# Kernel tuning notes

Hardware: AMD Instinct MI355X
Metric: run time of the kernel (lower is better)

The kernel has to match this reference:

```python
import jax, jax.numpy as jnp
import numpy as np

B, CL, QL, D2 = 64, 1024, 128, 512  # batch, c_len, q_len, hidden_size*2


def setup_inputs() -> dict:
    key = jax.random.key(0)
    ks = jax.random.split(key, 6)
    scale = 1.0 / np.sqrt(D2)
    return {
        "c": jax.random.normal(ks[0], (B, CL, D2), jnp.float32),
        "q": jax.random.normal(ks[1], (B, QL, D2), jnp.float32),
        "w_c": jax.random.normal(ks[2], (D2,), jnp.float32) * scale,
        "b_c": jnp.zeros((1,), jnp.float32),
        "w_q": jax.random.normal(ks[3], (D2,), jnp.float32) * scale,
        "b_q": jnp.zeros((1,), jnp.float32),
        "w_cq": jax.random.normal(ks[4], (D2,), jnp.float32) * scale,
        "b_cq": jnp.zeros((1,), jnp.float32),
    }


def reference(c, q, w_c, b_c, w_q, b_q, w_cq, b_cq):
    # BiDAF trilinear similarity.
    # Source loops over q_len: att_weight_cq(c * q_i); equivalent to
    # cq[b,i,j] = sum_d c[b,i,d] * q[b,j,d] * w_cq[d] + b_cq  -> single batched matmul.
    s_c = c @ w_c + b_c  # [B, CL]
    s_q = q @ w_q + b_q  # [B, QL]
    cq = jnp.einsum("bid,bjd->bij", c * w_cq, q) + b_cq  # [B, CL, QL]
    s = s_c[:, :, None] + s_q[:, None, :] + cq  # [B, CL, QL]
    a = jax.nn.softmax(s, axis=2)
    c2q = jnp.einsum("bij,bjd->bid", a, q)  # context-to-query attention
    b_att = jax.nn.softmax(jnp.max(s, axis=2), axis=1)  # [B, CL]
    q2c = jnp.einsum("bi,bid->bd", b_att, c)[:, None, :]  # [B, 1, D2], broadcast over CL
    x = jnp.concatenate([c, c2q, c * c2q, c * q2c], axis=-1)  # [B, CL, 8H]
    return x
```

## Files before the change

kernel.cpp:

```cpp
#include <hip/hip_runtime.h>

using bf16x8 = __attribute__((ext_vector_type(8))) short;
using f32x4  = __attribute__((ext_vector_type(4))) float;

#define NB 64
#define CLN 1024
#define QLN 128
#define DDN 512

typedef __attribute__((address_space(1))) const void GAS;
typedef __attribute__((address_space(3))) void LAS;

__device__ __forceinline__ unsigned short f2bf(float x){
    union { float f; unsigned u; } v; v.f = x;
    unsigned r = v.u + 0x7FFFu + ((v.u >> 16) & 1u);
    return (unsigned short)(r >> 16);
}
__device__ __forceinline__ float bf2f(unsigned short u){
    union { unsigned u; float f; } v; v.u = ((unsigned)u) << 16; return v.f;
}

__global__ __launch_bounds__(256) void k0_qprep(const float* __restrict__ q,
        unsigned short* __restrict__ qT, unsigned short* __restrict__ qbf){
    __shared__ float tile[QLN][65];
    const int b  = blockIdx.x;
    const int d0 = blockIdx.y * 64;
    const int t  = threadIdx.x;
    {
        const int col = t & 63, rg = t >> 6;
        #pragma unroll 4
        for (int p = 0; p < 32; ++p){
            int j = p*4 + rg;
            float v = q[(size_t)(b*QLN + j)*DDN + d0 + col];
            tile[j][col] = v;
            qbf[(size_t)(b*QLN + j)*DDN + d0 + col] = f2bf(v);
        }
    }
    __syncthreads();
    {
        const int j = t & 127, dg = t >> 7;
        #pragma unroll 4
        for (int p = 0; p < 32; ++p){
            int dd = p*2 + dg;
            qT[(size_t)(b*DDN + d0 + dd)*QLN + j] = f2bf(tile[j][dd]);
        }
    }
}

__global__ __launch_bounds__(256) void k0b_sq(const float* __restrict__ q,
        const float* __restrict__ w_q, float* __restrict__ sq){
    const int b = blockIdx.x;
    const int t = threadIdx.x;
    const int wave = t >> 6, lane = t & 63;
    float wv[8];
    #pragma unroll
    for (int e=0;e<8;++e) wv[e] = w_q[lane*8+e];
    for (int j = wave; j < QLN; j += 4){
        const float* qr = q + (size_t)(b*QLN + j)*DDN + lane*8;
        float s = 0.f;
        #pragma unroll
        for (int e=0;e<8;++e) s += qr[e]*wv[e];
        #pragma unroll
        for (int m=1;m<64;m<<=1) s += __shfl_xor(s, m, 64);
        if (lane==0) sq[b*QLN + j] = s;
    }
}

__global__ __launch_bounds__(256) void k0c_cprep(const float* __restrict__ c,
        const float* __restrict__ w_c, const float* __restrict__ w_cq,
        float* out, float* __restrict__ sc_ws, float* __restrict__ inv_ws){
    const int t = threadIdx.x, lane = t & 63, w = t >> 6;
    const int row0 = blockIdx.x*32 + w*8;
    float4 wc0 = *(const float4*)(w_c  + lane*8);
    float4 wc1 = *(const float4*)(w_c  + lane*8 + 4);
    float4 wq0 = *(const float4*)(w_cq + lane*8);
    float4 wq1 = *(const float4*)(w_cq + lane*8 + 4);
    #pragma unroll 2
    for (int p=0;p<8;++p){
        const size_t gi = (size_t)(row0 + p);
        const float* cr = c + gi*DDN + lane*8;
        f32x4 a  = *(const f32x4*)cr;
        f32x4 bb = *(const f32x4*)(cr+4);
        float s = a.x*wc0.x + a.y*wc0.y + a.z*wc0.z + a.w*wc0.w
                + bb.x*wc1.x + bb.y*wc1.y + bb.z*wc1.z + bb.w*wc1.w;
        #pragma unroll
        for (int m=1;m<64;m<<=1) s += __shfl_xor(s, m, 64);
        float* orow = out + gi*2048;
        __builtin_nontemporal_store(a,  (f32x4*)(orow + lane*8));
        __builtin_nontemporal_store(bb, (f32x4*)(orow + lane*8 + 4));
        uint4 pk;
        pk.x = (unsigned)f2bf(a.x*wq0.x)  | ((unsigned)f2bf(a.y*wq0.y)  << 16);
        pk.y = (unsigned)f2bf(a.z*wq0.z)  | ((unsigned)f2bf(a.w*wq0.w)  << 16);
        pk.z = (unsigned)f2bf(bb.x*wq1.x) | ((unsigned)f2bf(bb.y*wq1.y) << 16);
        pk.w = (unsigned)f2bf(bb.z*wq1.z) | ((unsigned)f2bf(bb.w*wq1.w) << 16);
        *(uint4*)((unsigned short*)(orow + 1792) + lane*8) = pk;
        if (lane==0) sc_ws[gi] = s;
    }
    if (blockIdx.x == 0){
        for (int d=t; d<DDN; d+=256){
            float wv = w_cq[d];
            inv_ws[d] = (fabsf(wv) > 1e-35f) ? 1.0f/wv : 0.0f;
        }
    }
}

__device__ __forceinline__ void stage_tile(const float* out, size_t girow0, int kc,
        unsigned short* buf, int wm, int lane){
    const int rsub = lane >> 3, c16 = lane & 7;
    #pragma unroll
    for (int r=0;r<4;++r){
        const int chunk = wm*4 + r;
        const int row   = chunk*8 + rsub;
        const int col16 = c16 ^ (row & 7);
        const unsigned short* g =
            (const unsigned short*)(out + (girow0 + row)*2048 + 1792) + kc*64 + col16*8;
        __builtin_amdgcn_global_load_lds((GAS*)g, (LAS*)(buf + chunk*512), 16, 0, 0);
    }
}

__global__ __launch_bounds__(256,3) void k1_main(
        float* out, const unsigned short* __restrict__ qbf,
        const unsigned short* __restrict__ qT, const float* __restrict__ sq_ws,
        const float* __restrict__ sc_ws, const float* __restrict__ inv_ws,
        float* __restrict__ vts, float* __restrict__ Mts, float* __restrict__ Sts){
    __shared__ unsigned short sm_u[16384];
    __shared__ float sm_vw[4][512];
    __shared__ float sm_sc[128], sm_sq[128], sm_m[128], sm_red[8];

    const int bid  = blockIdx.x;
    const int swzb = (bid & 7)*64 + (bid >> 3);
    const int b    = swzb >> 3;
    const int tile = swzb & 7;
    const int i0   = tile * 128;
    const int t    = threadIdx.x;
    const int lane = t & 63;
    const int wm   = t >> 6;
    const int l15  = lane & 15;
    const int l4   = lane >> 4;
    const size_t girow0 = (size_t)(b*CLN + i0);

    if (t < 128){ sm_sc[t] = sc_ws[girow0 + t]; sm_sq[t] = sq_ws[b*QLN + t]; }

    f32x4 acc[2][8];
    #pragma unroll
    for (int mi=0;mi<2;++mi)
        #pragma unroll
        for (int ni=0;ni<8;++ni) acc[mi][ni] = f32x4{0.f,0.f,0.f,0.f};

    stage_tile(out, girow0, 0, sm_u, wm, lane);
    __syncthreads();
    const unsigned short* qbbase = qbf + (size_t)b*QLN*DDN;
    for (int kc=0; kc<8; ++kc){
        const int cur = kc & 1;
        if (kc < 7) stage_tile(out, girow0, kc+1, sm_u + (cur^1)*8192, wm, lane);
        const char* abase = (const char*)sm_u + cur*16384;
        #pragma unroll
        for (int ks=0; ks<2; ++ks){
            const int kk2 = (ks*32 + l4*8)*2;
            bf16x8 af[2], bfr[8];
            #pragma unroll
            for (int mi=0;mi<2;++mi){
                const int row = wm*32 + mi*16 + l15;
                af[mi] = *(const bf16x8*)(abase + row*128 + (kk2 ^ ((row&7)<<4)));
            }
            #pragma unroll
            for (int ni=0;ni<8;++ni)
                bfr[ni] = *(const bf16x8*)(qbbase + (size_t)(ni*16+l15)*DDN + kc*64 + ks*32 + l4*8);
            #pragma unroll
            for (int mi=0;mi<2;++mi)
                #pragma unroll
                for (int ni=0;ni<8;++ni)
                    acc[mi][ni] = __builtin_amdgcn_mfma_f32_16x16x32_bf16(af[mi], bfr[ni], acc[mi][ni], 0,0,0);
        }
        __syncthreads();
    }

    float sqv[8];
    #pragma unroll
    for (int ni=0;ni<8;++ni) sqv[ni] = sm_sq[ni*16 + l15];
    #pragma unroll
    for (int mi=0;mi<2;++mi){
        #pragma unroll
        for (int r=0;r<4;++r){
            float rmax = -1e30f;
            #pragma unroll
            for (int ni=0;ni<8;++ni){
                float v = acc[mi][ni][r] + sqv[ni];
                acc[mi][ni][r] = v;
                rmax = fmaxf(rmax, v);
            }
            #pragma unroll
            for (int m=1;m<16;m<<=1) rmax = fmaxf(rmax, __shfl_xor(rmax, m, 64));
            const int iloc = wm*32 + mi*16 + l4*4 + r;
            if (l15 == 0) sm_m[iloc] = sm_sc[iloc] + rmax;
            float rsum = 0.f;
            #pragma unroll
            for (int ni=0;ni<8;++ni){
                float pv = __expf(acc[mi][ni][r] - rmax);
                acc[mi][ni][r] = pv;
                rsum += pv;
            }
            #pragma unroll
            for (int m=1;m<16;m<<=1) rsum += __shfl_xor(rsum, m, 64);
            const float inv = 1.f / rsum;
            #pragma unroll
            for (int ni=0;ni<8;++ni){
                const int colb = (ni*16 + l15)*2;
                *(unsigned short*)((char*)sm_u + iloc*256 + (colb ^ ((iloc&7)<<4)))
                    = f2bf(acc[mi][ni][r] * inv);
            }
        }
    }
    __syncthreads();

    float e0 = -1e30f;
    if (t < 128) e0 = sm_m[t];
    float v0 = e0;
    #pragma unroll
    for (int m=1;m<64;m<<=1) v0 = fmaxf(v0, __shfl_xor(v0, m, 64));
    if (lane==0) sm_red[wm] = v0;
    __syncthreads();
    const float mt = fmaxf(sm_red[0], sm_red[1]);
    float es = (t < 128) ? __expf(sm_m[t] - mt) : 0.f;
    #pragma unroll
    for (int m=1;m<64;m<<=1) es += __shfl_xor(es, m, 64);
    if (lane==0) sm_red[4+wm] = es;
    __syncthreads();
    const float St = sm_red[4]+sm_red[5]+sm_red[6]+sm_red[7];

    float wrow[2][4];
    #pragma unroll
    for (int mi=0;mi<2;++mi)
        #pragma unroll
        for (int r=0;r<4;++r)
            wrow[mi][r] = __expf(sm_m[wm*32 + mi*16 + l4*4 + r] - mt);
    #pragma unroll
    for (int k=0;k<8;++k) sm_vw[wm][lane + k*64] = 0.f;

    const unsigned short* qtbase = qT + (size_t)b*DDN*QLN;
    for (int dc=0; dc<4; ++dc){
        f32x4 acc2[2][8];
        #pragma unroll
        for (int mi=0;mi<2;++mi)
            #pragma unroll
            for (int ni=0;ni<8;++ni) acc2[mi][ni] = f32x4{0.f,0.f,0.f,0.f};
        #pragma unroll
        for (int jh=0; jh<2; ++jh){
            #pragma unroll
            for (int ks=0; ks<2; ++ks){
                const int kkp2 = (jh*64 + ks*32 + l4*8)*2;
                bf16x8 af[2], bfr[8];
                #pragma unroll
                for (int mi=0;mi<2;++mi){
                    const int row = wm*32 + mi*16 + l15;
                    af[mi] = *(const bf16x8*)((const char*)sm_u + row*256 + (kkp2 ^ ((row&7)<<4)));
                }
                #pragma unroll
                for (int ni=0;ni<8;++ni)
                    bfr[ni] = *(const bf16x8*)(qtbase + (size_t)(dc*128 + ni*16 + l15)*QLN + jh*64 + ks*32 + l4*8);
                #pragma unroll
                for (int mi=0;mi<2;++mi)
                    #pragma unroll
                    for (int ni=0;ni<8;++ni)
                        acc2[mi][ni] = __builtin_amdgcn_mfma_f32_16x16x32_bf16(af[mi], bfr[ni], acc2[mi][ni], 0,0,0);
            }
        }
        float invw[8];
        #pragma unroll
        for (int ni=0;ni<8;++ni) invw[ni] = inv_ws[dc*128 + ni*16 + l15];
        float vpart[8];
        #pragma unroll
        for (int ni=0;ni<8;++ni) vpart[ni] = 0.f;
        #pragma unroll
        for (int mi=0;mi<2;++mi){
            #pragma unroll
            for (int r=0;r<4;++r){
                const int rl = wm*32 + mi*16 + l4*4 + r;
                const unsigned short* cb =
                    (const unsigned short*)(out + (girow0 + rl)*2048 + 1792) + dc*128;
                float* orow = out + (girow0 + rl)*2048;
                const float wgt = wrow[mi][r];
                #pragma unroll
                for (int ni=0;ni<8;++ni){
                    const int dl = ni*16 + l15;
                    const float cv = bf2f(cb[dl]) * invw[ni];
                    const float v  = acc2[mi][ni][r];
                    __builtin_nontemporal_store(v,    orow + 512  + dc*128 + dl);
                    __builtin_nontemporal_store(cv*v, orow + 1024 + dc*128 + dl);
                    vpart[ni] += wgt * cv;
                }
            }
        }
        #pragma unroll
        for (int ni=0;ni<8;++ni){
            float v = vpart[ni];
            v += __shfl_xor(v, 16, 64);
            v += __shfl_xor(v, 32, 64);
            if (l4 == 0) sm_vw[wm][dc*128 + ni*16 + l15] = v;
        }
    }
    __syncthreads();
    for (int d=t; d<DDN; d+=256){
        float v = sm_vw[0][d] + sm_vw[1][d] + sm_vw[2][d] + sm_vw[3][d];
        vts[(size_t)(b*8 + tile)*DDN + d] = v;
    }
    if (t == 0){ Mts[b*8 + tile] = mt; Sts[b*8 + tile] = St; }
}

__global__ __launch_bounds__(256) void k2_combine(const float* __restrict__ vts,
        const float* __restrict__ Mts, const float* __restrict__ Sts,
        float* __restrict__ q2c){
    const int b = blockIdx.x, t = threadIdx.x;
    float Mt[8]; float M = -1e30f;
    #pragma unroll
    for (int i=0;i<8;++i){ Mt[i] = Mts[b*8+i]; M = fmaxf(M, Mt[i]); }
    float coef[8]; float denom = 0.f;
    #pragma unroll
    for (int i=0;i<8;++i){ coef[i] = __expf(Mt[i]-M); denom += coef[i]*Sts[b*8+i]; }
    const float inv = 1.f/denom;
    for (int d=t; d<DDN; d+=256){
        float s = 0.f;
        #pragma unroll
        for (int i=0;i<8;++i) s += coef[i]*vts[(size_t)(b*8+i)*DDN + d];
        q2c[b*DDN + d] = s*inv;
    }
}

__global__ __launch_bounds__(256) void k3_cq2c(float* out,
        const float* __restrict__ q2c, const float* __restrict__ inv_ws){
    const int t = threadIdx.x;
    const int rloc = t >> 6, ch = t & 63;
    for (int pass=0; pass<8; ++pass){
        const size_t rb = (size_t)blockIdx.x + (size_t)pass*2048;
        const size_t gi = rb*4 + rloc;
        const int b = (int)(gi >> 10);
        const unsigned short* cb = (const unsigned short*)(out + gi*2048 + 1792) + ch*8;
        uint4 raw = *(const uint4*)cb;
        const float* qp = q2c + b*DDN + ch*8;
        float4 qa = *(const float4*)qp;
        float4 qb = *(const float4*)(qp+4);
        const float* ip = inv_ws + ch*8;
        float4 ia = *(const float4*)ip;
        float4 ib = *(const float4*)(ip+4);
        f32x4 o0, o1;
        o0.x = bf2f((unsigned short)(raw.x & 0xffff)) * ia.x * qa.x;
        o0.y = bf2f((unsigned short)(raw.x >> 16))    * ia.y * qa.y;
        o0.z = bf2f((unsigned short)(raw.y & 0xffff)) * ia.z * qa.z;
        o0.w = bf2f((unsigned short)(raw.y >> 16))    * ia.w * qa.w;
        o1.x = bf2f((unsigned short)(raw.z & 0xffff)) * ib.x * qb.x;
        o1.y = bf2f((unsigned short)(raw.z >> 16))    * ib.y * qb.y;
        o1.z = bf2f((unsigned short)(raw.w & 0xffff)) * ib.z * qb.z;
        o1.w = bf2f((unsigned short)(raw.w >> 16))    * ib.w * qb.w;
        __syncthreads();
        f32x4* wp = (f32x4*)(out + gi*2048 + 1536) + ch*2;
        __builtin_nontemporal_store(o0, wp);
        __builtin_nontemporal_store(o1, wp+1);
    }
}

extern "C" void kernel_launch(void* const* d_in, const int* in_sizes, int n_in,
                              void* d_out, int out_size, void* d_ws, size_t ws_size,
                              hipStream_t stream) {
    const float* c    = (const float*)d_in[0];
    const float* q    = (const float*)d_in[1];
    const float* w_c  = (const float*)d_in[2];
    const float* w_q  = (const float*)d_in[4];
    const float* w_cq = (const float*)d_in[6];
    float* out = (float*)d_out;

    char* ws = (char*)d_ws;
    unsigned short* qT  = (unsigned short*)ws;
    unsigned short* qbf = (unsigned short*)(ws + 8388608);
    float* sq  = (float*)(ws + 16777216);
    float* sc  = (float*)(ws + 16777216 + 32768);
    float* inv = (float*)(ws + 16777216 + 32768 + 262144);
    float* Mts = (float*)(ws + 16777216 + 32768 + 262144 + 2048);
    float* Sts = (float*)(ws + 16777216 + 32768 + 262144 + 4096);
    float* vts = (float*)(ws + 16777216 + 32768 + 262144 + 6144);
    float* q2c = (float*)(ws + 16777216 + 32768 + 262144 + 6144 + 1048576);

    k0_qprep<<<dim3(NB, 8), 256, 0, stream>>>(q, qT, qbf);
    k0b_sq<<<NB, 256, 0, stream>>>(q, w_q, sq);
    k0c_cprep<<<2048, 256, 0, stream>>>(c, w_c, w_cq, out, sc, inv);
    k1_main<<<NB*8, 256, 0, stream>>>(out, qbf, qT, sq, sc, inv, vts, Mts, Sts);
    k2_combine<<<NB, 256, 0, stream>>>(vts, Mts, Sts, q2c);
    k3_cq2c<<<2048, 256, 0, stream>>>(out, q2c, inv);
}
```

Measured before the change: 266.2 us.

## Fuse context prep into main attention kernel and read fp32 c directly

Removes the separate c-prep kernel: the main kernel now loads fp32 c rows itself, computes the c·w_c score and the bf16 c*w_cq tile in registers, and writes them into LDS with double buffering. The bf16 scratch stash in the output buffer and the reciprocal-weight reconstruction go away. The c2q epilogue reads c exactly in fp32 and also writes the c slice of the output. The final q2c kernel reads fp32 c from the output and uses a flat grid-stride loop. MFMA operand order is swapped so epilogue stores are vectorised float4, at the cost of lower occupancy (launch bound 2) and more LDS.

```diff
diff --git a/kernel.cpp b/kernel.cpp
--- a/kernel.cpp
+++ b/kernel.cpp
@@ -11,10 +11,10 @@
 typedef __attribute__((address_space(1))) const void GAS;
 typedef __attribute__((address_space(3))) void LAS;
 
-__device__ __forceinline__ unsigned short f2bf(float x){
+__device__ __forceinline__ unsigned f2bf(float x){
     union { float f; unsigned u; } v; v.f = x;
     unsigned r = v.u + 0x7FFFu + ((v.u >> 16) & 1u);
-    return (unsigned short)(r >> 16);
+    return r >> 16;
 }
 __device__ __forceinline__ float bf2f(unsigned short u){
     union { unsigned u; float f; } v; v.u = ((unsigned)u) << 16; return v.f;
@@ -33,7 +33,7 @@
             int j = p*4 + rg;
             float v = q[(size_t)(b*QLN + j)*DDN + d0 + col];
             tile[j][col] = v;
-            qbf[(size_t)(b*QLN + j)*DDN + d0 + col] = f2bf(v);
+            qbf[(size_t)(b*QLN + j)*DDN + d0 + col] = (unsigned short)f2bf(v);
         }
     }
     __syncthreads();
@@ -42,7 +42,7 @@
         #pragma unroll 4
         for (int p = 0; p < 32; ++p){
             int dd = p*2 + dg;
-            qT[(size_t)(b*DDN + d0 + dd)*QLN + j] = f2bf(tile[j][dd]);
+            qT[(size_t)(b*DDN + d0 + dd)*QLN + j] = (unsigned short)f2bf(tile[j][dd]);
         }
     }
 }
@@ -66,66 +66,17 @@
     }
 }
 
-__global__ __launch_bounds__(256) void k0c_cprep(const float* __restrict__ c,
+__global__ __launch_bounds__(256,2) void k1_main(
+        const float* __restrict__ c, const unsigned short* __restrict__ qbf,
+        const unsigned short* __restrict__ qT, const float* __restrict__ sq_ws,
         const float* __restrict__ w_c, const float* __restrict__ w_cq,
-        float* out, float* __restrict__ sc_ws, float* __restrict__ inv_ws){
-    const int t = threadIdx.x, lane = t & 63, w = t >> 6;
-    const int row0 = blockIdx.x*32 + w*8;
-    float4 wc0 = *(const float4*)(w_c  + lane*8);
-    float4 wc1 = *(const float4*)(w_c  + lane*8 + 4);
-    float4 wq0 = *(const float4*)(w_cq + lane*8);
-    float4 wq1 = *(const float4*)(w_cq + lane*8 + 4);
-    #pragma unroll 2
-    for (int p=0;p<8;++p){
-        const size_t gi = (size_t)(row0 + p);
-        const float* cr = c + gi*DDN + lane*8;
-        f32x4 a  = *(const f32x4*)cr;
-        f32x4 bb = *(const f32x4*)(cr+4);
-        float s = a.x*wc0.x + a.y*wc0.y + a.z*wc0.z + a.w*wc0.w
-                + bb.x*wc1.x + bb.y*wc1.y + bb.z*wc1.z + bb.w*wc1.w;
-        #pragma unroll
-        for (int m=1;m<64;m<<=1) s += __shfl_xor(s, m, 64);
-        float* orow = out + gi*2048;
-        __builtin_nontemporal_store(a,  (f32x4*)(orow + lane*8));
-        __builtin_nontemporal_store(bb, (f32x4*)(orow + lane*8 + 4));
-        uint4 pk;
-        pk.x = (unsigned)f2bf(a.x*wq0.x)  | ((unsigned)f2bf(a.y*wq0.y)  << 16);
-        pk.y = (unsigned)f2bf(a.z*wq0.z)  | ((unsigned)f2bf(a.w*wq0.w)  << 16);
-        pk.z = (unsigned)f2bf(bb.x*wq1.x) | ((unsigned)f2bf(bb.y*wq1.y) << 16);
-        pk.w = (unsigned)f2bf(bb.z*wq1.z) | ((unsigned)f2bf(bb.w*wq1.w) << 16);
-        *(uint4*)((unsigned short*)(orow + 1792) + lane*8) = pk;
-        if (lane==0) sc_ws[gi] = s;
-    }
-    if (blockIdx.x == 0){
-        for (int d=t; d<DDN; d+=256){
-            float wv = w_cq[d];
-            inv_ws[d] = (fabsf(wv) > 1e-35f) ? 1.0f/wv : 0.0f;
-        }
-    }
-}
-
-__device__ __forceinline__ void stage_tile(const float* out, size_t girow0, int kc,
-        unsigned short* buf, int wm, int lane){
-    const int rsub = lane >> 3, c16 = lane & 7;
-    #pragma unroll
-    for (int r=0;r<4;++r){
-        const int chunk = wm*4 + r;
-        const int row   = chunk*8 + rsub;
-        const int col16 = c16 ^ (row & 7);
-        const unsigned short* g =
-            (const unsigned short*)(out + (girow0 + row)*2048 + 1792) + kc*64 + col16*8;
-        __builtin_amdgcn_global_load_lds((GAS*)g, (LAS*)(buf + chunk*512), 16, 0, 0);
-    }
-}
-
-__global__ __launch_bounds__(256,3) void k1_main(
-        float* out, const unsigned short* __restrict__ qbf,
-        const unsigned short* __restrict__ qT, const float* __restrict__ sq_ws,
-        const float* __restrict__ sc_ws, const float* __restrict__ inv_ws,
+        float* __restrict__ out,
         float* __restrict__ vts, float* __restrict__ Mts, float* __restrict__ Sts){
     __shared__ unsigned short sm_u[16384];
-    __shared__ float sm_vw[4][512];
-    __shared__ float sm_sc[128], sm_sq[128], sm_m[128], sm_red[8];
+    __shared__ float sm_vw[16][512];
+    __shared__ float sm_wc[512], sm_wq[512];
+    __shared__ float sm_sq[128], sm_m[128], sm_wrow[128], sm_sc[128];
+    __shared__ float sm_scp[256], sm_red[8];
 
     const int bid  = blockIdx.x;
     const int swzb = (bid & 7)*64 + (bid >> 3);
@@ -139,172 +90,201 @@
     const int l4   = lane >> 4;
     const size_t girow0 = (size_t)(b*CLN + i0);
 
-    if (t < 128){ sm_sc[t] = sc_ws[girow0 + t]; sm_sq[t] = sq_ws[b*QLN + t]; }
+    if (t < 128) sm_sq[t] = sq_ws[b*QLN + t];
+    sm_wc[t]     = w_c[t];   sm_wc[t+256] = w_c[t+256];
+    sm_wq[t]     = w_cq[t];  sm_wq[t+256] = w_cq[t+256];
+
+    const int srow = t >> 1, shalf = t & 1;
+    const float* crow = c + (girow0 + srow)*DDN + shalf*32;
+    float scp = 0.f;
+
+    f32x4 ld[8];
+    #pragma unroll
+    for (int e=0;e<8;++e) ld[e] = *(const f32x4*)(crow + e*4);
+    __syncthreads();
+
+    #define DO_STAGE(KC, BUF) do {                                            \
+        const int dbase = (KC)*64 + shalf*32;                                 \
+        _Pragma("unroll")                                                     \
+        for (int q8=0; q8<4; ++q8){                                           \
+            f32x4 v0 = ld[q8*2], v1 = ld[q8*2+1];                             \
+            f32x4 wq0 = *(const f32x4*)(sm_wq + dbase + q8*8);                \
+            f32x4 wq1 = *(const f32x4*)(sm_wq + dbase + q8*8 + 4);            \
+            f32x4 wc0 = *(const f32x4*)(sm_wc + dbase + q8*8);                \
+            f32x4 wc1 = *(const f32x4*)(sm_wc + dbase + q8*8 + 4);            \
+            scp += v0.x*wc0.x + v0.y*wc0.y + v0.z*wc0.z + v0.w*wc0.w          \
+                 + v1.x*wc1.x + v1.y*wc1.y + v1.z*wc1.z + v1.w*wc1.w;         \
+            uint4 pk;                                                         \
+            pk.x = f2bf(v0.x*wq0.x) | (f2bf(v0.y*wq0.y) << 16);               \
+            pk.y = f2bf(v0.z*wq0.z) | (f2bf(v0.w*wq0.w) << 16);               \
+            pk.z = f2bf(v1.x*wq1.x) | (f2bf(v1.y*wq1.y) << 16);               \
+            pk.w = f2bf(v1.z*wq1.z) | (f2bf(v1.w*wq1.w) << 16);               \
+            *(uint4*)((char*)(BUF) + srow*128 +                               \
+                      ((shalf*64 + q8*16) ^ ((srow&7)<<4))) = pk;             \
+        }                                                                     \
+    } while(0)
+
+    DO_STAGE(0, sm_u);
+    __syncthreads();
 
     f32x4 acc[2][8];
     #pragma unroll
     for (int mi=0;mi<2;++mi)
         #pragma unroll
-        for (int ni=0;ni<8;++ni) acc[mi][ni] = f32x4{0.f,0.f,0.f,0.f};
-
-    stage_tile(out, girow0, 0, sm_u, wm, lane);
-    __syncthreads();
+        for (int nj=0;nj<8;++nj) acc[mi][nj] = f32x4{0.f,0.f,0.f,0.f};
+
     const unsigned short* qbbase = qbf + (size_t)b*QLN*DDN;
     for (int kc=0; kc<8; ++kc){
-        const int cur = kc & 1;
-        if (kc < 7) stage_tile(out, girow0, kc+1, sm_u + (cur^1)*8192, wm, lane);
-        const char* abase = (const char*)sm_u + cur*16384;
+        unsigned short* bufc = sm_u + (kc&1)*8192;
+        unsigned short* bufn = sm_u + ((kc&1)^1)*8192;
+        if (kc < 7){
+            const float* crn = crow + (kc+1)*64;
+            #pragma unroll
+            for (int e=0;e<8;++e) ld[e] = *(const f32x4*)(crn + e*4);
+        }
         #pragma unroll
         for (int ks=0; ks<2; ++ks){
-            const int kk2 = (ks*32 + l4*8)*2;
             bf16x8 af[2], bfr[8];
             #pragma unroll
             for (int mi=0;mi<2;++mi){
                 const int row = wm*32 + mi*16 + l15;
-                af[mi] = *(const bf16x8*)(abase + row*128 + (kk2 ^ ((row&7)<<4)));
-            }
-            #pragma unroll
-            for (int ni=0;ni<8;++ni)
-                bfr[ni] = *(const bf16x8*)(qbbase + (size_t)(ni*16+l15)*DDN + kc*64 + ks*32 + l4*8);
+                af[mi] = *(const bf16x8*)((char*)bufc + row*128 + ((ks*64 + l4*16) ^ ((row&7)<<4)));
+            }
+            #pragma unroll
+            for (int nj=0;nj<8;++nj)
+                bfr[nj] = *(const bf16x8*)(qbbase + (size_t)(nj*16+l15)*DDN + kc*64 + ks*32 + l4*8);
             #pragma unroll
             for (int mi=0;mi<2;++mi)
                 #pragma unroll
-                for (int ni=0;ni<8;++ni)
-                    acc[mi][ni] = __builtin_amdgcn_mfma_f32_16x16x32_bf16(af[mi], bfr[ni], acc[mi][ni], 0,0,0);
-        }
+                for (int nj=0;nj<8;++nj)
+                    acc[mi][nj] = __builtin_amdgcn_mfma_f32_16x16x32_bf16(bfr[nj], af[mi], acc[mi][nj], 0,0,0);
+        }
+        if (kc < 7) DO_STAGE(kc+1, bufn);
         __syncthreads();
     }
 
-    float sqv[8];
-    #pragma unroll
-    for (int ni=0;ni<8;++ni) sqv[ni] = sm_sq[ni*16 + l15];
+    sm_scp[t] = scp;
+    __syncthreads();
+    if (t < 128) sm_sc[t] = sm_scp[2*t] + sm_scp[2*t+1];
+    __syncthreads();
+
+    f32x4 sq4[8];
+    #pragma unroll
+    for (int nj=0;nj<8;++nj) sq4[nj] = *(const f32x4*)(sm_sq + nj*16 + l4*4);
+
     #pragma unroll
     for (int mi=0;mi<2;++mi){
-        #pragma unroll
-        for (int r=0;r<4;++r){
-            float rmax = -1e30f;
-            #pragma unroll
-            for (int ni=0;ni<8;++ni){
-                float v = acc[mi][ni][r] + sqv[ni];
-                acc[mi][ni][r] = v;
+        const int irow = wm*32 + mi*16 + l15;
+        float rmax = -1e30f;
+        #pragma unroll
+        for (int nj=0;nj<8;++nj){
+            #pragma unroll
+            for (int r=0;r<4;++r){
+                float v = acc[mi][nj][r] + sq4[nj][r];
+                acc[mi][nj][r] = v;
                 rmax = fmaxf(rmax, v);
             }
-            #pragma unroll
-            for (int m=1;m<16;m<<=1) rmax = fmaxf(rmax, __shfl_xor(rmax, m, 64));
-            const int iloc = wm*32 + mi*16 + l4*4 + r;
-            if (l15 == 0) sm_m[iloc] = sm_sc[iloc] + rmax;
-            float rsum = 0.f;
-            #pragma unroll
-            for (int ni=0;ni<8;++ni){
-                float pv = __expf(acc[mi][ni][r] - rmax);
-                acc[mi][ni][r] = pv;
+        }
+        rmax = fmaxf(rmax, __shfl_xor(rmax, 16, 64));
+        rmax = fmaxf(rmax, __shfl_xor(rmax, 32, 64));
+        if (l4 == 0) sm_m[irow] = sm_sc[irow] + rmax;
+        float rsum = 0.f;
+        #pragma unroll
+        for (int nj=0;nj<8;++nj){
+            #pragma unroll
+            for (int r=0;r<4;++r){
+                float pv = __expf(acc[mi][nj][r] - rmax);
+                acc[mi][nj][r] = pv;
                 rsum += pv;
             }
-            #pragma unroll
-            for (int m=1;m<16;m<<=1) rsum += __shfl_xor(rsum, m, 64);
-            const float inv = 1.f / rsum;
-            #pragma unroll
-            for (int ni=0;ni<8;++ni){
-                const int colb = (ni*16 + l15)*2;
-                *(unsigned short*)((char*)sm_u + iloc*256 + (colb ^ ((iloc&7)<<4)))
-                    = f2bf(acc[mi][ni][r] * inv);
-            }
-        }
-    }
-    __syncthreads();
-
-    float e0 = -1e30f;
-    if (t < 128) e0 = sm_m[t];
-    float v0 = e0;
+        }
+        rsum += __shfl_xor(rsum, 16, 64);
+        rsum += __shfl_xor(rsum, 32, 64);
+        const float inv = 1.f / rsum;
+        #pragma unroll
+        for (int nj=0;nj<8;++nj){
+            uint2 u;
+            u.x = f2bf(acc[mi][nj][0]*inv) | (f2bf(acc[mi][nj][1]*inv) << 16);
+            u.y = f2bf(acc[mi][nj][2]*inv) | (f2bf(acc[mi][nj][3]*inv) << 16);
+            *(uint2*)((char*)sm_u + irow*256 + ((nj*32 + l4*8) ^ ((irow&7)<<4))) = u;
+        }
+    }
+    __syncthreads();
+
+    float v0 = (t < 128) ? sm_m[t] : -1e30f;
     #pragma unroll
     for (int m=1;m<64;m<<=1) v0 = fmaxf(v0, __shfl_xor(v0, m, 64));
     if (lane==0) sm_red[wm] = v0;
     __syncthreads();
     const float mt = fmaxf(sm_red[0], sm_red[1]);
-    float es = (t < 128) ? __expf(sm_m[t] - mt) : 0.f;
+    float ev = (t < 128) ? __expf(sm_m[t] - mt) : 0.f;
+    if (t < 128) sm_wrow[t] = ev;
+    float es = ev;
     #pragma unroll
     for (int m=1;m<64;m<<=1) es += __shfl_xor(es, m, 64);
     if (lane==0) sm_red[4+wm] = es;
     __syncthreads();
     const float St = sm_red[4]+sm_red[5]+sm_red[6]+sm_red[7];
-
-    float wrow[2][4];
-    #pragma unroll
-    for (int mi=0;mi<2;++mi)
-        #pragma unroll
-        for (int r=0;r<4;++r)
-            wrow[mi][r] = __expf(sm_m[wm*32 + mi*16 + l4*4 + r] - mt);
-    #pragma unroll
-    for (int k=0;k<8;++k) sm_vw[wm][lane + k*64] = 0.f;
+    float wrow_reg[2];
+    wrow_reg[0] = sm_wrow[wm*32 + l15];
+    wrow_reg[1] = sm_wrow[wm*32 + 16 + l15];
 
     const unsigned short* qtbase = qT + (size_t)b*DDN*QLN;
     for (int dc=0; dc<4; ++dc){
-        f32x4 acc2[2][8];
-        #pragma unroll
-        for (int mi=0;mi<2;++mi)
-            #pragma unroll
-            for (int ni=0;ni<8;++ni) acc2[mi][ni] = f32x4{0.f,0.f,0.f,0.f};
-        #pragma unroll
-        for (int jh=0; jh<2; ++jh){
-            #pragma unroll
-            for (int ks=0; ks<2; ++ks){
-                const int kkp2 = (jh*64 + ks*32 + l4*8)*2;
-                bf16x8 af[2], bfr[8];
-                #pragma unroll
-                for (int mi=0;mi<2;++mi){
-                    const int row = wm*32 + mi*16 + l15;
-                    af[mi] = *(const bf16x8*)((const char*)sm_u + row*256 + (kkp2 ^ ((row&7)<<4)));
-                }
-                #pragma unroll
-                for (int ni=0;ni<8;++ni)
-                    bfr[ni] = *(const bf16x8*)(qtbase + (size_t)(dc*128 + ni*16 + l15)*QLN + jh*64 + ks*32 + l4*8);
+        f32x4 acc2[8][2];
+        #pragma unroll
+        for (int dt=0;dt<8;++dt){ acc2[dt][0] = f32x4{0,0,0,0}; acc2[dt][1] = f32x4{0,0,0,0}; }
+        #pragma unroll
+        for (int jc=0; jc<4; ++jc){
+            bf16x8 a2[8], b2[2];
+            #pragma unroll
+            for (int dt=0;dt<8;++dt)
+                a2[dt] = *(const bf16x8*)(qtbase + (size_t)(dc*128 + dt*16 + l15)*QLN + jc*32 + l4*8);
+            #pragma unroll
+            for (int mi=0;mi<2;++mi){
+                const int irow = wm*32 + mi*16 + l15;
+                b2[mi] = *(const bf16x8*)((char*)sm_u + irow*256 + ((jc*64 + l4*16) ^ ((irow&7)<<4)));
+            }
+            #pragma unroll
+            for (int dt=0;dt<8;++dt)
                 #pragma unroll
                 for (int mi=0;mi<2;++mi)
-                    #pragma unroll
-                    for (int ni=0;ni<8;++ni)
-                        acc2[mi][ni] = __builtin_amdgcn_mfma_f32_16x16x32_bf16(af[mi], bfr[ni], acc2[mi][ni], 0,0,0);
-            }
-        }
-        float invw[8];
-        #pragma unroll
-        for (int ni=0;ni<8;++ni) invw[ni] = inv_ws[dc*128 + ni*16 + l15];
-        float vpart[8];
-        #pragma unroll
-        for (int ni=0;ni<8;++ni) vpart[ni] = 0.f;
-        #pragma unroll
-        for (int mi=0;mi<2;++mi){
-            #pragma unroll
-            for (int r=0;r<4;++r){
-                const int rl = wm*32 + mi*16 + l4*4 + r;
-                const unsigned short* cb =
-                    (const unsigned short*)(out + (girow0 + rl)*2048 + 1792) + dc*128;
-                float* orow = out + (girow0 + rl)*2048;
-                const float wgt = wrow[mi][r];
-                #pragma unroll
-                for (int ni=0;ni<8;++ni){
-                    const int dl = ni*16 + l15;
-                    const float cv = bf2f(cb[dl]) * invw[ni];
-                    const float v  = acc2[mi][ni][r];
-                    __builtin_nontemporal_store(v,    orow + 512  + dc*128 + dl);
-                    __builtin_nontemporal_store(cv*v, orow + 1024 + dc*128 + dl);
-                    vpart[ni] += wgt * cv;
-                }
-            }
-        }
-        #pragma unroll
-        for (int ni=0;ni<8;++ni){
-            float v = vpart[ni];
-            v += __shfl_xor(v, 16, 64);
-            v += __shfl_xor(v, 32, 64);
-            if (l4 == 0) sm_vw[wm][dc*128 + ni*16 + l15] = v;
+                    acc2[dt][mi] = __builtin_amdgcn_mfma_f32_16x16x32_bf16(a2[dt], b2[mi], acc2[dt][mi], 0,0,0);
+        }
+        #pragma unroll
+        for (int dt=0; dt<8; ++dt){
+            const int d0 = dc*128 + dt*16 + l4*4;
+            f32x4 vp = f32x4{0,0,0,0};
+            #pragma unroll
+            for (int mi=0; mi<2; ++mi){
+                const int irow = wm*32 + mi*16 + l15;
+                const size_t gi = girow0 + irow;
+                f32x4 cv = *(const f32x4*)(c + gi*DDN + d0);
+                f32x4 v  = acc2[dt][mi];
+                float* orow = out + gi*2048;
+                __builtin_nontemporal_store(cv, (f32x4*)(orow + d0));
+                __builtin_nontemporal_store(v,  (f32x4*)(orow + 512 + d0));
+                f32x4 cq; cq.x=cv.x*v.x; cq.y=cv.y*v.y; cq.z=cv.z*v.z; cq.w=cv.w*v.w;
+                __builtin_nontemporal_store(cq, (f32x4*)(orow + 1024 + d0));
+                const float w = wrow_reg[mi];
+                vp.x += w*cv.x; vp.y += w*cv.y; vp.z += w*cv.z; vp.w += w*cv.w;
+            }
+            vp.x += __shfl_xor(vp.x, 4, 64); vp.y += __shfl_xor(vp.y, 4, 64);
+            vp.z += __shfl_xor(vp.z, 4, 64); vp.w += __shfl_xor(vp.w, 4, 64);
+            vp.x += __shfl_xor(vp.x, 8, 64); vp.y += __shfl_xor(vp.y, 8, 64);
+            vp.z += __shfl_xor(vp.z, 8, 64); vp.w += __shfl_xor(vp.w, 8, 64);
+            if (l15 < 4) *(f32x4*)(&sm_vw[wm*4 + l15][d0]) = vp;
         }
     }
     __syncthreads();
     for (int d=t; d<DDN; d+=256){
-        float v = sm_vw[0][d] + sm_vw[1][d] + sm_vw[2][d] + sm_vw[3][d];
-        vts[(size_t)(b*8 + tile)*DDN + d] = v;
+        float s = 0.f;
+        #pragma unroll
+        for (int s16=0;s16<16;++s16) s += sm_vw[s16][d];
+        vts[(size_t)(b*8 + tile)*DDN + d] = s;
     }
     if (t == 0){ Mts[b*8 + tile] = mt; Sts[b*8 + tile] = St; }
+    #undef DO_STAGE
 }
 
 __global__ __launch_bounds__(256) void k2_combine(const float* __restrict__ vts,
@@ -326,35 +306,16 @@
     }
 }
 
-__global__ __launch_bounds__(256) void k3_cq2c(float* out,
-        const float* __restrict__ q2c, const float* __restrict__ inv_ws){
-    const int t = threadIdx.x;
-    const int rloc = t >> 6, ch = t & 63;
-    for (int pass=0; pass<8; ++pass){
-        const size_t rb = (size_t)blockIdx.x + (size_t)pass*2048;
-        const size_t gi = rb*4 + rloc;
-        const int b = (int)(gi >> 10);
-        const unsigned short* cb = (const unsigned short*)(out + gi*2048 + 1792) + ch*8;
-        uint4 raw = *(const uint4*)cb;
-        const float* qp = q2c + b*DDN + ch*8;
-        float4 qa = *(const float4*)qp;
-        float4 qb = *(const float4*)(qp+4);
-        const float* ip = inv_ws + ch*8;
-        float4 ia = *(const float4*)ip;
-        float4 ib = *(const float4*)(ip+4);
-        f32x4 o0, o1;
-        o0.x = bf2f((unsigned short)(raw.x & 0xffff)) * ia.x * qa.x;
-        o0.y = bf2f((unsigned short)(raw.x >> 16))    * ia.y * qa.y;
-        o0.z = bf2f((unsigned short)(raw.y & 0xffff)) * ia.z * qa.z;
-        o0.w = bf2f((unsigned short)(raw.y >> 16))    * ia.w * qa.w;
-        o1.x = bf2f((unsigned short)(raw.z & 0xffff)) * ib.x * qb.x;
-        o1.y = bf2f((unsigned short)(raw.z >> 16))    * ib.y * qb.y;
-        o1.z = bf2f((unsigned short)(raw.w & 0xffff)) * ib.z * qb.z;
-        o1.w = bf2f((unsigned short)(raw.w >> 16))    * ib.w * qb.w;
-        __syncthreads();
-        f32x4* wp = (f32x4*)(out + gi*2048 + 1536) + ch*2;
-        __builtin_nontemporal_store(o0, wp);
-        __builtin_nontemporal_store(o1, wp+1);
+__global__ __launch_bounds__(256) void k3_cq2c(float* out, const float* __restrict__ q2c){
+    const int total = NB*CLN*(DDN/4);
+    for (int idx = blockIdx.x*256 + threadIdx.x; idx < total; idx += gridDim.x*256){
+        const int d4 = idx & 127;
+        const int gi = idx >> 7;
+        const int b  = gi >> 10;
+        f32x4 cv = *(const f32x4*)(out + (size_t)gi*2048 + d4*4);
+        f32x4 qv = *(const f32x4*)(q2c + b*DDN + d4*4);
+        f32x4 o; o.x=cv.x*qv.x; o.y=cv.y*qv.y; o.z=cv.z*qv.z; o.w=cv.w*qv.w;
+        __builtin_nontemporal_store(o, (f32x4*)(out + (size_t)gi*2048 + 1536 + d4*4));
     }
 }
 
@@ -372,17 +333,14 @@
     unsigned short* qT  = (unsigned short*)ws;
     unsigned short* qbf = (unsigned short*)(ws + 8388608);
     float* sq  = (float*)(ws + 16777216);
-    float* sc  = (float*)(ws + 16777216 + 32768);
-    float* inv = (float*)(ws + 16777216 + 32768 + 262144);
-    float* Mts = (float*)(ws + 16777216 + 32768 + 262144 + 2048);
-    float* Sts = (float*)(ws + 16777216 + 32768 + 262144 + 4096);
-    float* vts = (float*)(ws + 16777216 + 32768 + 262144 + 6144);
-    float* q2c = (float*)(ws + 16777216 + 32768 + 262144 + 6144 + 1048576);
+    float* Mts = (float*)(ws + 16777216 + 32768);
+    float* Sts = (float*)(ws + 16777216 + 32768 + 2048);
+    float* vts = (float*)(ws + 16777216 + 32768 + 4096);
+    float* q2c = (float*)(ws + 16777216 + 32768 + 4096 + 1048576);
 
     k0_qprep<<<dim3(NB, 8), 256, 0, stream>>>(q, qT, qbf);
     k0b_sq<<<NB, 256, 0, stream>>>(q, w_q, sq);
-    k0c_cprep<<<2048, 256, 0, stream>>>(c, w_c, w_cq, out, sc, inv);
-    k1_main<<<NB*8, 256, 0, stream>>>(out, qbf, qT, sq, sc, inv, vts, Mts, Sts);
+    k1_main<<<NB*8, 256, 0, stream>>>(c, qbf, qT, sq, w_c, w_cq, out, vts, Mts, Sts);
     k2_combine<<<NB, 256, 0, stream>>>(vts, Mts, Sts, q2c);
-    k3_cq2c<<<2048, 256, 0, stream>>>(out, q2c, inv);
-}
+    k3_cq2c<<<2048, 256, 0, stream>>>(out, q2c);
+}
```

After: 285.6 us. 7.3% more time.
